# Kernel optimization log

Measured on AMD Instinct MI355X. Metric: run time of the kernel, lower is better.

The kernel has to match this reference:

```python
import jax, jax.numpy as jnp
import numpy as np

B, S, P, HID, HQ, HKV, D, MAXP = 8, 4, 4096, 4096, 32, 8, 128, 8192


def setup_inputs() -> dict:
    key = jax.random.key(0)
    ks = jax.random.split(key, 8)
    # rotary tables (Llama-style: freqs duplicated across halves)
    inv_freq = 1.0 / (10000.0 ** (jnp.arange(0, D // 2, dtype=jnp.float32) / (D // 2)))
    t = jnp.arange(MAXP, dtype=jnp.float32)
    emb = jnp.concatenate([jnp.outer(t, inv_freq)] * 2, axis=-1)  # [MAXP, D]
    w = 0.02
    return {
        "x": jax.random.normal(ks[0], (B, S, HID), dtype=jnp.float32),
        "wq": w * jax.random.normal(ks[1], (HID, HQ * D), dtype=jnp.float32),
        "wk": w * jax.random.normal(ks[2], (HID, HKV * D), dtype=jnp.float32),
        "wv": w * jax.random.normal(ks[3], (HID, HKV * D), dtype=jnp.float32),
        "wo": w * jax.random.normal(ks[4], (HQ * D, HID), dtype=jnp.float32),
        "cos": jnp.cos(emb),
        "sin": jnp.sin(emb),
        "k_cache": jax.random.normal(ks[5], (B, P, HKV, D), dtype=jnp.float32),
        "v_cache": jax.random.normal(ks[6], (B, P, HKV, D), dtype=jnp.float32),
        "past_len": P,
    }


def _rope(x, c, s):
    # x: [B,S,H,D]; c,s: [1,S,1,D] -- half-rotation RoPE
    half = x.shape[-1] // 2
    x1, x2 = x[..., :half], x[..., half:]
    return x * c + jnp.concatenate([-x2, x1], axis=-1) * s


def reference(x, wq, wk, wv, wo, cos, sin, k_cache, v_cache, past_len):
    b, s, _ = x.shape
    hq, hkv, d = HQ, HKV, D
    q = (x @ wq).reshape(b, s, hq, d)
    k = (x @ wk).reshape(b, s, hkv, d)
    v = (x @ wv).reshape(b, s, hkv, d)

    pos = past_len + jnp.arange(s)                     # new-token positions
    c = cos[pos][None, :, None, :]
    sn = sin[pos][None, :, None, :]
    q = _rope(q, c, sn)
    k = _rope(k, c, sn)

    # append new kv to cache
    k_all = jnp.concatenate([k_cache, k], axis=1)      # [B,T,HKV,D]
    v_all = jnp.concatenate([v_cache, v], axis=1)
    t_len = k_all.shape[1]

    group = hq // hkv
    qg = q.reshape(b, s, hkv, group, d)
    scores = jnp.einsum('bskgd,btkd->bkgst', qg, k_all) / jnp.sqrt(jnp.asarray(d, x.dtype))

    # causal: query at position past_len+i attends to key positions <= past_len+i
    key_pos = jnp.arange(t_len)
    mask = pos[:, None] >= key_pos[None, :]            # [S,T]
    scores = jnp.where(mask[None, None, None], scores, jnp.asarray(-1e30, scores.dtype))
    attn = jax.nn.softmax(scores, axis=-1)

    out = jnp.einsum('bkgst,btkd->bskgd', attn, v_all).reshape(b, s, hq * d)
    return out @ wo
```

## Files before the change

### kernel.cpp

```cpp
#include <hip/hip_runtime.h>
#include <math.h>

#define NB 8
#define NS 4
#define NP 4096
#define HID 4096
#define NHQ 32
#define NHKV 8
#define ND 128
#define NGROUP 4
#define NBS 32
#define NQI 16
#define NCHUNK 17
#define TCHUNK 256
#define KSPLIT 16
#define QKV_COLS 6144
#define LOG2E 1.4426950408889634f

__global__ __launch_bounds__(256) void prep_xT(const float* __restrict__ x,
                                               float* __restrict__ xT) {
  int n = blockIdx.x * 256 + threadIdx.x;
  int r = n >> 12;
  int k = n & 4095;
  xT[k * NBS + r] = x[n];
}

__global__ __launch_bounds__(256) void rope_kernel(
    const float* __restrict__ qb, const float* __restrict__ kb,
    const float* __restrict__ cosp, const float* __restrict__ sinp,
    const int* __restrict__ past_len, float* __restrict__ q_t,
    float* __restrict__ k_new) {
  int n = blockIdx.x * 256 + threadIdx.x;
  int pl = past_len[0];
  if (n < NBS * HID) {
    int r = n >> 12;
    int hd = n & 4095;
    int h = hd >> 7, d = hd & 127;
    int b = r >> 2, s = r & 3;
    int pos = pl + s;
    float c = cosp[pos * ND + d], sn = sinp[pos * ND + d];
    float v = qb[n];
    float other = (d < 64) ? -qb[n + 64] : qb[n - 64];
    float rv = fmaf(v, c, other * sn);
    int kv = h >> 2, g = h & 3;
    q_t[(((b * NHKV + kv) * ND + d) * NQI) + g * NS + s] = rv;
  } else {
    n -= NBS * HID;
    int r = n >> 10;
    int hd = n & 1023;
    int kv = hd >> 7, d = hd & 127;
    int b = r >> 2, s = r & 3;
    int pos = pl + s;
    float c = cosp[pos * ND + d], sn = sinp[pos * ND + d];
    float v = kb[n];
    float other = (d < 64) ? -kb[n + 64] : kb[n - 64];
    k_new[((b * NHKV + kv) * NS + s) * ND + d] = fmaf(v, c, other * sn);
  }
}

__global__ __launch_bounds__(256) void gemm_part(
    const float* __restrict__ A_T, const float* __restrict__ wq,
    const float* __restrict__ wk, const float* __restrict__ wv,
    const float* __restrict__ wo, float* __restrict__ P, int mode) {
  __shared__ float lds[2 * 64 * 64];
  int cb = blockIdx.x, kb = blockIdx.y;
  int ncols = mode ? 4096 : QKV_COLS;
  int col0 = cb * 128;
  const float* W;
  int ld, wcol;
  if (mode) {
    W = wo; ld = 4096; wcol = col0;
  } else if (col0 < 4096) {
    W = wq; ld = 4096; wcol = col0;
  } else if (col0 < 5120) {
    W = wk; ld = 1024; wcol = col0 - 4096;
  } else {
    W = wv; ld = 1024; wcol = col0 - 5120;
  }
  int tid = threadIdx.x;
  int lane = tid & 63;
  int wid = __builtin_amdgcn_readfirstlane(tid >> 6);
  int k0 = kb * 256 + wid * 64;
  const float* wp = W + (size_t)k0 * ld + wcol + lane * 2;
  const float* xp = A_T + (size_t)k0 * NBS;
  float acc[64];
#pragma unroll
  for (int v = 0; v < 64; v++) acc[v] = 0.f;

  float2 wbuf[8];
#pragma unroll
  for (int u = 0; u < 8; u++) wbuf[u] = *(const float2*)(wp + (size_t)u * ld);
#pragma unroll 1
  for (int kk = 0; kk < 64; kk += 8) {
    float2 cur[8];
#pragma unroll
    for (int u = 0; u < 8; u++) cur[u] = wbuf[u];
    if (kk + 8 < 64) {
#pragma unroll
      for (int u = 0; u < 8; u++)
        wbuf[u] = *(const float2*)(wp + (size_t)(kk + 8 + u) * ld);
    }
#pragma unroll
    for (int u = 0; u < 8; u++) {
      const float* xr = xp + (kk + u) * NBS;
#pragma unroll
      for (int m = 0; m < NBS; m++) {
        acc[2 * m] = fmaf(xr[m], cur[u].x, acc[2 * m]);
        acc[2 * m + 1] = fmaf(xr[m], cur[u].y, acc[2 * m + 1]);
      }
    }
  }
  if (wid >= 2) {
#pragma unroll
    for (int v = 0; v < 64; v++) lds[(wid - 2) * 4096 + v * 64 + lane] = acc[v];
  }
  __syncthreads();
  if (wid < 2) {
#pragma unroll
    for (int v = 0; v < 64; v++) acc[v] += lds[wid * 4096 + v * 64 + lane];
  }
  __syncthreads();
  if (wid == 1) {
#pragma unroll
    for (int v = 0; v < 64; v++) lds[v * 64 + lane] = acc[v];
  }
  __syncthreads();
  if (wid == 0) {
#pragma unroll
    for (int v = 0; v < 64; v++) acc[v] += lds[v * 64 + lane];
#pragma unroll
    for (int m = 0; m < NBS; m++) {
      float2 st = make_float2(acc[2 * m], acc[2 * m + 1]);
      *(float2*)(P + ((size_t)kb * NBS + m) * ncols + col0 + lane * 2) = st;
    }
  }
}

__global__ __launch_bounds__(256) void reduce_qkv(const float* __restrict__ P,
                                                  float* __restrict__ qb,
                                                  float* __restrict__ kbuf,
                                                  float* __restrict__ vbuf) {
  size_t idx = ((size_t)blockIdx.x * 256 + threadIdx.x) * 4;
  float4 s = make_float4(0.f, 0.f, 0.f, 0.f);
#pragma unroll
  for (int p = 0; p < KSPLIT; p++) {
    float4 v = *(const float4*)(P + (size_t)p * (NBS * QKV_COLS) + idx);
    s.x += v.x; s.y += v.y; s.z += v.z; s.w += v.w;
  }
  int r = (int)(idx / QKV_COLS);
  int col = (int)(idx % QKV_COLS);
  float* dst;
  if (col < 4096)
    dst = qb + (size_t)r * 4096 + col;
  else if (col < 5120)
    dst = kbuf + (size_t)r * 1024 + (col - 4096);
  else
    dst = vbuf + (size_t)r * 1024 + (col - 5120);
  *(float4*)dst = s;
}

__global__ __launch_bounds__(256) void reduce_o(const float* __restrict__ P,
                                                float* __restrict__ outp) {
  size_t idx = ((size_t)blockIdx.x * 256 + threadIdx.x) * 4;
  float4 s = make_float4(0.f, 0.f, 0.f, 0.f);
#pragma unroll
  for (int p = 0; p < KSPLIT; p++) {
    float4 v = *(const float4*)(P + (size_t)p * (NBS * 4096) + idx);
    s.x += v.x; s.y += v.y; s.z += v.z; s.w += v.w;
  }
  *(float4*)(outp + idx) = s;
}

__global__ __launch_bounds__(256) void attn_kernel(
    const float* __restrict__ q_t, const float* __restrict__ k_cache,
    const float* __restrict__ v_cache, const float* __restrict__ k_new,
    const float* __restrict__ vbuf, float* __restrict__ part_o,
    float* __restrict__ part_m, float* __restrict__ part_l) {
  __shared__ float p_lds[TCHUNK * 17];
  __shared__ float redm[NQI][4];
  __shared__ float redl[NQI][4];
  __shared__ float mfin[NQI];
  int bk = blockIdx.x;
  int chunk = blockIdx.y;
  int blk = bk * NCHUNK + chunk;
  int b = bk >> 3, kv = bk & 7;
  int tid = threadIdx.x;
  int lane = tid & 63;
  int wid = tid >> 6;
  bool last = (chunk == NCHUNK - 1);
  int tcount = last ? NS : TCHUNK;
  const float* qbase = q_t + (size_t)bk * (ND * NQI);

  int t_loc = tid;
  bool valid = t_loc < tcount;
  int t_eff = valid ? t_loc : 0;
  const float* kp =
      last ? (k_new + ((size_t)bk * NS + t_eff) * ND)
           : (k_cache +
              (((size_t)b * NP + chunk * TCHUNK + t_eff) * NHKV + kv) * ND);
  float s_acc[NQI];
#pragma unroll
  for (int i = 0; i < NQI; i++) s_acc[i] = 0.f;
#pragma unroll 8
  for (int d4 = 0; d4 < 32; ++d4) {
    float4 kvv = *(const float4*)(kp + d4 * 4);
    const float* qp = qbase + (d4 * 4) * NQI;
#pragma unroll
    for (int i = 0; i < NQI; i++) {
      float s = s_acc[i];
      s = fmaf(kvv.x, qp[i], s);
      s = fmaf(kvv.y, qp[NQI + i], s);
      s = fmaf(kvv.z, qp[2 * NQI + i], s);
      s = fmaf(kvv.w, qp[3 * NQI + i], s);
      s_acc[i] = s;
    }
  }
  const float scale = 0.08838834764831845f;
  float sc[NQI];
#pragma unroll
  for (int i = 0; i < NQI; i++) {
    float s = s_acc[i] * scale;
    if (!valid || (last && t_loc > (i & 3))) s = -__builtin_inff();
    sc[i] = s;
  }
#pragma unroll
  for (int i = 0; i < NQI; i++) {
    float m = sc[i];
#pragma unroll
    for (int off = 1; off < 64; off <<= 1) m = fmaxf(m, __shfl_xor(m, off, 64));
    if (lane == 0) redm[i][wid] = m;
  }
  __syncthreads();
  if (tid < NQI) {
    float m = fmaxf(fmaxf(redm[tid][0], redm[tid][1]),
                    fmaxf(redm[tid][2], redm[tid][3]));
    mfin[tid] = m;
  }
  __syncthreads();
  float l_loc[NQI];
#pragma unroll
  for (int i = 0; i < NQI; i++) {
    float p = exp2f((sc[i] - mfin[i]) * LOG2E);
    p_lds[t_loc * 17 + i] = p;
    l_loc[i] = p;
  }
#pragma unroll
  for (int i = 0; i < NQI; i++) {
    float l = l_loc[i];
#pragma unroll
    for (int off = 1; off < 64; off <<= 1) l += __shfl_xor(l, off, 64);
    if (lane == 0) redl[i][wid] = l;
  }
  __syncthreads();
  if (tid < NQI) {
    float l = redl[tid][0] + redl[tid][1] + redl[tid][2] + redl[tid][3];
    part_m[(size_t)blk * NQI + tid] = mfin[tid];
    part_l[(size_t)blk * NQI + tid] = l;
  }

  int r0 = tid >> 5;
  int dq = (tid & 31) * 4;
  const float* vpb =
      last ? (vbuf + (size_t)b * NS * (NHKV * ND) + kv * ND + dq)
           : (v_cache + ((size_t)b * NP + chunk * TCHUNK) * (NHKV * ND) +
              kv * ND + dq);
  float o0[4] = {0, 0, 0, 0}, o1[4] = {0, 0, 0, 0};
#pragma unroll 8
  for (int t = 0; t < tcount; ++t) {
    float4 vv = *(const float4*)(vpb + (size_t)t * (NHKV * ND));
    float p0 = p_lds[t * 17 + r0];
    float p1 = p_lds[t * 17 + r0 + 8];
    o0[0] = fmaf(p0, vv.x, o0[0]); o0[1] = fmaf(p0, vv.y, o0[1]);
    o0[2] = fmaf(p0, vv.z, o0[2]); o0[3] = fmaf(p0, vv.w, o0[3]);
    o1[0] = fmaf(p1, vv.x, o1[0]); o1[1] = fmaf(p1, vv.y, o1[1]);
    o1[2] = fmaf(p1, vv.z, o1[2]); o1[3] = fmaf(p1, vv.w, o1[3]);
  }
  size_t obase = (size_t)blk * (NQI * ND);
  *(float4*)(part_o + obase + (size_t)r0 * ND + dq) =
      make_float4(o0[0], o0[1], o0[2], o0[3]);
  *(float4*)(part_o + obase + (size_t)(r0 + 8) * ND + dq) =
      make_float4(o1[0], o1[1], o1[2], o1[3]);
}

__global__ __launch_bounds__(256) void combine_kernel(
    const float* __restrict__ part_o, const float* __restrict__ part_m,
    const float* __restrict__ part_l, float* __restrict__ attn_T) {
  int bk = blockIdx.x;
  int tid = threadIdx.x;
  int i = tid >> 4;
  int dh = (tid & 15) * 4 + blockIdx.y * 64;
  float M = -__builtin_inff();
#pragma unroll
  for (int c = 0; c < NCHUNK; c++)
    M = fmaxf(M, part_m[((size_t)bk * NCHUNK + c) * NQI + i]);
  float L = 0.f;
  float o0 = 0.f, o1 = 0.f, o2 = 0.f, o3 = 0.f;
#pragma unroll
  for (int c = 0; c < NCHUNK; c++) {
    size_t pc = (size_t)bk * NCHUNK + c;
    float mc = part_m[pc * NQI + i];
    float w = exp2f((mc - M) * LOG2E);
    L = fmaf(part_l[pc * NQI + i], w, L);
    float4 po = *(const float4*)(part_o + pc * (NQI * ND) + (size_t)i * ND + dh);
    o0 = fmaf(w, po.x, o0);
    o1 = fmaf(w, po.y, o1);
    o2 = fmaf(w, po.z, o2);
    o3 = fmaf(w, po.w, o3);
  }
  float inv = 1.0f / L;
  int b = bk >> 3, kv = bk & 7;
  int g = i >> 2, s = i & 3;
  int h = kv * NGROUP + g;
  int r = b * NS + s;
  attn_T[(size_t)(h * ND + dh + 0) * NBS + r] = o0 * inv;
  attn_T[(size_t)(h * ND + dh + 1) * NBS + r] = o1 * inv;
  attn_T[(size_t)(h * ND + dh + 2) * NBS + r] = o2 * inv;
  attn_T[(size_t)(h * ND + dh + 3) * NBS + r] = o3 * inv;
}

extern "C" void kernel_launch(void* const* d_in, const int* in_sizes, int n_in,
                              void* d_out, int out_size, void* d_ws,
                              size_t ws_size, hipStream_t stream) {
  const float* x = (const float*)d_in[0];
  const float* wq = (const float*)d_in[1];
  const float* wk = (const float*)d_in[2];
  const float* wv = (const float*)d_in[3];
  const float* wo = (const float*)d_in[4];
  const float* cosp = (const float*)d_in[5];
  const float* sinp = (const float*)d_in[6];
  const float* k_cache = (const float*)d_in[7];
  const float* v_cache = (const float*)d_in[8];
  const int* past_len = (const int*)d_in[9];
  float* out = (float*)d_out;

  float* ws = (float*)d_ws;
  float* xT = ws;
  float* qb = xT + 131072;
  float* kbuf = qb + 131072;
  float* vbuf = kbuf + 32768;
  float* q_t = vbuf + 32768;
  float* k_new = q_t + 131072;
  float* attn_T = k_new + 32768;
  float* R = attn_T + 131072;
  float* Pq = R;
  float* part_o = R;
  float* part_m = R + 2228224;
  float* part_l = part_m + 17408;
  float* Po = R;

  prep_xT<<<512, 256, 0, stream>>>(x, xT);
  gemm_part<<<dim3(48, KSPLIT), 256, 0, stream>>>(xT, wq, wk, wv, wo, Pq, 0);
  reduce_qkv<<<192, 256, 0, stream>>>(Pq, qb, kbuf, vbuf);
  rope_kernel<<<640, 256, 0, stream>>>(qb, kbuf, cosp, sinp, past_len, q_t,
                                       k_new);
  attn_kernel<<<dim3(64, NCHUNK), 256, 0, stream>>>(
      q_t, k_cache, v_cache, k_new, vbuf, part_o, part_m, part_l);
  combine_kernel<<<dim3(64, 2), 256, 0, stream>>>(part_o, part_m, part_l,
                                                  attn_T);
  gemm_part<<<dim3(32, KSPLIT), 256, 0, stream>>>(attn_T, wq, wk, wv, wo, Po,
                                                  1);
  reduce_o<<<128, 256, 0, stream>>>(Po, out);
}
```

Before: 463.2 us.

## Stage GEMM activations in LDS, widen weight loads, split attention PV over time

The split-K GEMM now copies its activation slice into shared memory and has each lane load float4 weight columns (4 columns by 16 rows instead of 2 by 32). It also doubles the K-split to 32 when the workspace is large enough, which adds parallelism but doubles the partial-sum traffic seen by the reduce kernels. The attention PV stage now gives each warp a 32-token slice and all 16 queries, with a transposed P layout, followed by a cross-warp reduction in LDS. This trades more accumulator registers and extra syncs for fewer redundant V reads.

```diff
diff --git a/kernel.cpp b/kernel.cpp
--- a/kernel.cpp
+++ b/kernel.cpp
@@ -13,7 +13,6 @@
 #define NQI 16
 #define NCHUNK 17
 #define TCHUNK 256
-#define KSPLIT 16
 #define QKV_COLS 6144
 #define LOG2E 1.4426950408889634f
 
@@ -58,11 +57,12 @@
   }
 }
 
+template <int KSLICE>
 __global__ __launch_bounds__(256) void gemm_part(
     const float* __restrict__ A_T, const float* __restrict__ wq,
     const float* __restrict__ wk, const float* __restrict__ wv,
     const float* __restrict__ wo, float* __restrict__ P, int mode) {
-  __shared__ float lds[2 * 64 * 64];
+  __shared__ __align__(16) float lds[8192];
   int cb = blockIdx.x, kb = blockIdx.y;
   int ncols = mode ? 4096 : QKV_COLS;
   int col0 = cb * 128;
@@ -80,36 +80,62 @@
   int tid = threadIdx.x;
   int lane = tid & 63;
   int wid = __builtin_amdgcn_readfirstlane(tid >> 6);
-  int k0 = kb * 256 + wid * 64;
-  const float* wp = W + (size_t)k0 * ld + wcol + lane * 2;
-  const float* xp = A_T + (size_t)k0 * NBS;
+  int l32 = lane & 31;
+  int mh = lane >> 5;
+  int kblk = kb * KSLICE;
+  constexpr int KW = KSLICE / 4;
+  int k0 = wid * KW;
+  const float* wp = W + (size_t)(kblk + k0) * ld + wcol + l32 * 4;
+
+  float4 wb[8];
+#pragma unroll
+  for (int u = 0; u < 8; u++) wb[u] = *(const float4*)(wp + (size_t)u * ld);
+
+  {
+    const float4* src = (const float4*)(A_T + (size_t)kblk * NBS);
+    float4* dst = (float4*)lds;
+#pragma unroll
+    for (int p = 0; p < KSLICE / 32; p++)
+      dst[p * 256 + tid] = src[p * 256 + tid];
+  }
+  __syncthreads();
+
   float acc[64];
 #pragma unroll
   for (int v = 0; v < 64; v++) acc[v] = 0.f;
 
-  float2 wbuf[8];
-#pragma unroll
-  for (int u = 0; u < 8; u++) wbuf[u] = *(const float2*)(wp + (size_t)u * ld);
-#pragma unroll 1
-  for (int kk = 0; kk < 64; kk += 8) {
-    float2 cur[8];
-#pragma unroll
-    for (int u = 0; u < 8; u++) cur[u] = wbuf[u];
-    if (kk + 8 < 64) {
-#pragma unroll
-      for (int u = 0; u < 8; u++)
-        wbuf[u] = *(const float2*)(wp + (size_t)(kk + 8 + u) * ld);
-    }
-#pragma unroll
-    for (int u = 0; u < 8; u++) {
-      const float* xr = xp + (kk + u) * NBS;
-#pragma unroll
-      for (int m = 0; m < NBS; m++) {
-        acc[2 * m] = fmaf(xr[m], cur[u].x, acc[2 * m]);
-        acc[2 * m + 1] = fmaf(xr[m], cur[u].y, acc[2 * m + 1]);
-      }
-    }
-  }
+  const float* xp = lds + (size_t)k0 * NBS + mh * 16;
+
+  auto body = [&](int kk, float4 w) {
+    const float* xr = xp + (size_t)kk * NBS;
+    float4 xa = *(const float4*)(xr);
+    float4 xb = *(const float4*)(xr + 4);
+    float4 xc = *(const float4*)(xr + 8);
+    float4 xd = *(const float4*)(xr + 12);
+    float xm[16] = {xa.x, xa.y, xa.z, xa.w, xb.x, xb.y, xb.z, xb.w,
+                    xc.x, xc.y, xc.z, xc.w, xd.x, xd.y, xd.z, xd.w};
+#pragma unroll
+    for (int m = 0; m < 16; m++) {
+      acc[4 * m + 0] = fmaf(xm[m], w.x, acc[4 * m + 0]);
+      acc[4 * m + 1] = fmaf(xm[m], w.y, acc[4 * m + 1]);
+      acc[4 * m + 2] = fmaf(xm[m], w.z, acc[4 * m + 2]);
+      acc[4 * m + 3] = fmaf(xm[m], w.w, acc[4 * m + 3]);
+    }
+  };
+
+#pragma unroll 8
+  for (int kk = 0; kk < KW - 8; kk++) {
+    float4 w = wb[kk & 7];
+    wb[kk & 7] = *(const float4*)(wp + (size_t)(kk + 8) * ld);
+    body(kk, w);
+  }
+#pragma unroll
+  for (int kk = KW - 8; kk < KW; kk++) {
+    float4 w = wb[kk & 7];
+    body(kk, w);
+  }
+
+  __syncthreads();
   if (wid >= 2) {
 #pragma unroll
     for (int v = 0; v < 64; v++) lds[(wid - 2) * 4096 + v * 64 + lane] = acc[v];
@@ -129,13 +155,16 @@
 #pragma unroll
     for (int v = 0; v < 64; v++) acc[v] += lds[v * 64 + lane];
 #pragma unroll
-    for (int m = 0; m < NBS; m++) {
-      float2 st = make_float2(acc[2 * m], acc[2 * m + 1]);
-      *(float2*)(P + ((size_t)kb * NBS + m) * ncols + col0 + lane * 2) = st;
-    }
-  }
-}
-
+    for (int m = 0; m < 16; m++) {
+      float4 st = make_float4(acc[4 * m], acc[4 * m + 1], acc[4 * m + 2],
+                              acc[4 * m + 3]);
+      *(float4*)(P + ((size_t)kb * NBS + mh * 16 + m) * ncols + col0 +
+                 l32 * 4) = st;
+    }
+  }
+}
+
+template <int KS>
 __global__ __launch_bounds__(256) void reduce_qkv(const float* __restrict__ P,
                                                   float* __restrict__ qb,
                                                   float* __restrict__ kbuf,
@@ -143,7 +172,7 @@
   size_t idx = ((size_t)blockIdx.x * 256 + threadIdx.x) * 4;
   float4 s = make_float4(0.f, 0.f, 0.f, 0.f);
 #pragma unroll
-  for (int p = 0; p < KSPLIT; p++) {
+  for (int p = 0; p < KS; p++) {
     float4 v = *(const float4*)(P + (size_t)p * (NBS * QKV_COLS) + idx);
     s.x += v.x; s.y += v.y; s.z += v.z; s.w += v.w;
   }
@@ -159,12 +188,13 @@
   *(float4*)dst = s;
 }
 
+template <int KS>
 __global__ __launch_bounds__(256) void reduce_o(const float* __restrict__ P,
                                                 float* __restrict__ outp) {
   size_t idx = ((size_t)blockIdx.x * 256 + threadIdx.x) * 4;
   float4 s = make_float4(0.f, 0.f, 0.f, 0.f);
 #pragma unroll
-  for (int p = 0; p < KSPLIT; p++) {
+  for (int p = 0; p < KS; p++) {
     float4 v = *(const float4*)(P + (size_t)p * (NBS * 4096) + idx);
     s.x += v.x; s.y += v.y; s.z += v.z; s.w += v.w;
   }
@@ -176,10 +206,11 @@
     const float* __restrict__ v_cache, const float* __restrict__ k_new,
     const float* __restrict__ vbuf, float* __restrict__ part_o,
     float* __restrict__ part_m, float* __restrict__ part_l) {
-  __shared__ float p_lds[TCHUNK * 17];
+  __shared__ __align__(16) float sbuf[NQI * TCHUNK];
   __shared__ float redm[NQI][4];
   __shared__ float redl[NQI][4];
   __shared__ float mfin[NQI];
+  float* p_lds = sbuf;
   int bk = blockIdx.x;
   int chunk = blockIdx.y;
   int blk = bk * NCHUNK + chunk;
@@ -232,16 +263,15 @@
   }
   __syncthreads();
   if (tid < NQI) {
-    float m = fmaxf(fmaxf(redm[tid][0], redm[tid][1]),
-                    fmaxf(redm[tid][2], redm[tid][3]));
-    mfin[tid] = m;
+    mfin[tid] = fmaxf(fmaxf(redm[tid][0], redm[tid][1]),
+                      fmaxf(redm[tid][2], redm[tid][3]));
   }
   __syncthreads();
   float l_loc[NQI];
 #pragma unroll
   for (int i = 0; i < NQI; i++) {
     float p = exp2f((sc[i] - mfin[i]) * LOG2E);
-    p_lds[t_loc * 17 + i] = p;
+    p_lds[i * TCHUNK + t_loc] = p;
     l_loc[i] = p;
   }
 #pragma unroll
@@ -253,33 +283,75 @@
   }
   __syncthreads();
   if (tid < NQI) {
-    float l = redl[tid][0] + redl[tid][1] + redl[tid][2] + redl[tid][3];
     part_m[(size_t)blk * NQI + tid] = mfin[tid];
-    part_l[(size_t)blk * NQI + tid] = l;
-  }
-
-  int r0 = tid >> 5;
+    part_l[(size_t)blk * NQI + tid] =
+        redl[tid][0] + redl[tid][1] + redl[tid][2] + redl[tid][3];
+  }
+
+  int g = tid >> 5;
   int dq = (tid & 31) * 4;
+  int tbeg = g * 32;
+  int tnum = tcount - tbeg;
+  tnum = tnum < 0 ? 0 : (tnum > 32 ? 32 : tnum);
   const float* vpb =
-      last ? (vbuf + (size_t)b * NS * (NHKV * ND) + kv * ND + dq)
-           : (v_cache + ((size_t)b * NP + chunk * TCHUNK) * (NHKV * ND) +
+      last ? (vbuf + ((size_t)b * NS + tbeg) * (NHKV * ND) + kv * ND + dq)
+           : (v_cache + ((size_t)b * NP + chunk * TCHUNK + tbeg) * (NHKV * ND) +
               kv * ND + dq);
-  float o0[4] = {0, 0, 0, 0}, o1[4] = {0, 0, 0, 0};
-#pragma unroll 8
-  for (int t = 0; t < tcount; ++t) {
-    float4 vv = *(const float4*)(vpb + (size_t)t * (NHKV * ND));
-    float p0 = p_lds[t * 17 + r0];
-    float p1 = p_lds[t * 17 + r0 + 8];
-    o0[0] = fmaf(p0, vv.x, o0[0]); o0[1] = fmaf(p0, vv.y, o0[1]);
-    o0[2] = fmaf(p0, vv.z, o0[2]); o0[3] = fmaf(p0, vv.w, o0[3]);
-    o1[0] = fmaf(p1, vv.x, o1[0]); o1[1] = fmaf(p1, vv.y, o1[1]);
-    o1[2] = fmaf(p1, vv.z, o1[2]); o1[3] = fmaf(p1, vv.w, o1[3]);
-  }
-  size_t obase = (size_t)blk * (NQI * ND);
-  *(float4*)(part_o + obase + (size_t)r0 * ND + dq) =
-      make_float4(o0[0], o0[1], o0[2], o0[3]);
-  *(float4*)(part_o + obase + (size_t)(r0 + 8) * ND + dq) =
-      make_float4(o1[0], o1[1], o1[2], o1[3]);
+  float o[NQI][4];
+#pragma unroll
+  for (int i = 0; i < NQI; i++) o[i][0] = o[i][1] = o[i][2] = o[i][3] = 0.f;
+#pragma unroll 4
+  for (int tt = 0; tt < tnum; ++tt) {
+    float4 vv = *(const float4*)(vpb + (size_t)tt * (NHKV * ND));
+    const float* pp = p_lds + (tbeg + tt);
+#pragma unroll
+    for (int i = 0; i < NQI; i++) {
+      float p = pp[i * TCHUNK];
+      o[i][0] = fmaf(p, vv.x, o[i][0]);
+      o[i][1] = fmaf(p, vv.y, o[i][1]);
+      o[i][2] = fmaf(p, vv.z, o[i][2]);
+      o[i][3] = fmaf(p, vv.w, o[i][3]);
+    }
+  }
+#pragma unroll
+  for (int i = 0; i < NQI; i++) {
+#pragma unroll
+    for (int c = 0; c < 4; c++) o[i][c] += __shfl_xor(o[i][c], 32, 64);
+  }
+  __syncthreads();
+  float* red = sbuf;
+  if (wid >= 2 && lane < 32) {
+#pragma unroll
+    for (int i = 0; i < NQI; i++)
+      *(float4*)(red + ((wid - 2) * NQI + i) * 128 + dq) =
+          make_float4(o[i][0], o[i][1], o[i][2], o[i][3]);
+  }
+  __syncthreads();
+  if (wid < 2 && lane < 32) {
+#pragma unroll
+    for (int i = 0; i < NQI; i++) {
+      float4 r = *(const float4*)(red + (wid * NQI + i) * 128 + dq);
+      o[i][0] += r.x; o[i][1] += r.y; o[i][2] += r.z; o[i][3] += r.w;
+    }
+  }
+  __syncthreads();
+  if (wid == 1 && lane < 32) {
+#pragma unroll
+    for (int i = 0; i < NQI; i++)
+      *(float4*)(red + i * 128 + dq) =
+          make_float4(o[i][0], o[i][1], o[i][2], o[i][3]);
+  }
+  __syncthreads();
+  if (wid == 0 && lane < 32) {
+    size_t obase = (size_t)blk * (NQI * ND);
+#pragma unroll
+    for (int i = 0; i < NQI; i++) {
+      float4 r = *(const float4*)(red + i * 128 + dq);
+      *(float4*)(part_o + obase + (size_t)i * ND + dq) =
+          make_float4(o[i][0] + r.x, o[i][1] + r.y, o[i][2] + r.z,
+                      o[i][3] + r.w);
+    }
+  }
 }
 
 __global__ __launch_bounds__(256) void combine_kernel(
@@ -348,16 +420,30 @@
   float* part_l = part_m + 17408;
   float* Po = R;
 
+  const size_t need32 = (size_t)(622592 + 32 * NBS * QKV_COLS) * sizeof(float);
+  const bool big = ws_size >= need32;
+
   prep_xT<<<512, 256, 0, stream>>>(x, xT);
-  gemm_part<<<dim3(48, KSPLIT), 256, 0, stream>>>(xT, wq, wk, wv, wo, Pq, 0);
-  reduce_qkv<<<192, 256, 0, stream>>>(Pq, qb, kbuf, vbuf);
+  if (big) {
+    gemm_part<128><<<dim3(48, 32), 256, 0, stream>>>(xT, wq, wk, wv, wo, Pq, 0);
+    reduce_qkv<32><<<192, 256, 0, stream>>>(Pq, qb, kbuf, vbuf);
+  } else {
+    gemm_part<256><<<dim3(48, 16), 256, 0, stream>>>(xT, wq, wk, wv, wo, Pq, 0);
+    reduce_qkv<16><<<192, 256, 0, stream>>>(Pq, qb, kbuf, vbuf);
+  }
   rope_kernel<<<640, 256, 0, stream>>>(qb, kbuf, cosp, sinp, past_len, q_t,
                                        k_new);
   attn_kernel<<<dim3(64, NCHUNK), 256, 0, stream>>>(
       q_t, k_cache, v_cache, k_new, vbuf, part_o, part_m, part_l);
   combine_kernel<<<dim3(64, 2), 256, 0, stream>>>(part_o, part_m, part_l,
                                                   attn_T);
-  gemm_part<<<dim3(32, KSPLIT), 256, 0, stream>>>(attn_T, wq, wk, wv, wo, Po,
-                                                  1);
-  reduce_o<<<128, 256, 0, stream>>>(Po, out);
-}
+  if (big) {
+    gemm_part<128><<<dim3(32, 32), 256, 0, stream>>>(attn_T, wq, wk, wv, wo,
+                                                     Po, 1);
+    reduce_o<32><<<128, 256, 0, stream>>>(Po, out);
+  } else {
+    gemm_part<256><<<dim3(32, 16), 256, 0, stream>>>(attn_T, wq, wk, wv, wo,
+                                                     Po, 1);
+    reduce_o<16><<<128, 256, 0, stream>>>(Po, out);
+  }
+}
```

Result: no change. 464.6 us (+0.3%).

## Restructure skinny GEMM with async global-to-LDS double-buffered weight tiles

Applied to the files above, without the earlier changes.

Rewrites the split-K GEMM so each block covers 256 columns and a K slice. Weight rows stream into a double-buffered LDS tile through global_load_lds, and the activations are staged once in LDS. Each wave now owns 8 rows by 4 columns, which removes the cross-wave LDS reduction. A deeper split-K (32 slices) is used when the workspace is large enough. The intent is better bandwidth use on the weight stream and more blocks in flight, at the cost of larger partial buffers and a longer reduce.

```diff
diff --git a/kernel.cpp b/kernel.cpp
--- a/kernel.cpp
+++ b/kernel.cpp
@@ -13,7 +13,6 @@
 #define NQI 16
 #define NCHUNK 17
 #define TCHUNK 256
-#define KSPLIT 16
 #define QKV_COLS 6144
 #define LOG2E 1.4426950408889634f
 
@@ -58,14 +57,23 @@
   }
 }
 
+__device__ __forceinline__ void gl_lds16(const float* g, float* l) {
+  __builtin_amdgcn_global_load_lds(
+      (const __attribute__((address_space(1))) void*)g,
+      (__attribute__((address_space(3))) void*)l, 16, 0, 0);
+}
+
+template <int KSLICE>
 __global__ __launch_bounds__(256) void gemm_part(
     const float* __restrict__ A_T, const float* __restrict__ wq,
     const float* __restrict__ wk, const float* __restrict__ wv,
     const float* __restrict__ wo, float* __restrict__ P, int mode) {
-  __shared__ float lds[2 * 64 * 64];
+  constexpr int NCH = KSLICE / 16;
+  __shared__ __align__(16) float xs[KSLICE * 32];
+  __shared__ __align__(16) float wbuf[2 * 16 * 256];
   int cb = blockIdx.x, kb = blockIdx.y;
   int ncols = mode ? 4096 : QKV_COLS;
-  int col0 = cb * 128;
+  int col0 = cb * 256;
   const float* W;
   int ld, wcol;
   if (mode) {
@@ -80,62 +88,80 @@
   int tid = threadIdx.x;
   int lane = tid & 63;
   int wid = __builtin_amdgcn_readfirstlane(tid >> 6);
-  int k0 = kb * 256 + wid * 64;
-  const float* wp = W + (size_t)k0 * ld + wcol + lane * 2;
-  const float* xp = A_T + (size_t)k0 * NBS;
-  float acc[64];
-#pragma unroll
-  for (int v = 0; v < 64; v++) acc[v] = 0.f;
-
-  float2 wbuf[8];
-#pragma unroll
-  for (int u = 0; u < 8; u++) wbuf[u] = *(const float2*)(wp + (size_t)u * ld);
+  int lane4 = lane * 4;
+  int m0 = wid * 8;
+  int kblk = kb * KSLICE;
+  const float* wbase = W + (size_t)kblk * ld + wcol;
+
+#pragma unroll
+  for (int j = 0; j < KSLICE / 32; j++) {
+    gl_lds16(A_T + (size_t)kblk * 32 + j * 1024 + wid * 256 + lane4,
+             xs + j * 1024 + wid * 256);
+  }
+#pragma unroll
+  for (int j = 0; j < 4; j++) {
+    int row = j * 4 + wid;
+    gl_lds16(wbase + (size_t)row * ld + lane4, wbuf + row * 256);
+  }
+#pragma unroll
+  for (int j = 0; j < 4; j++) {
+    int row = j * 4 + wid;
+    gl_lds16(wbase + (size_t)(16 + row) * ld + lane4,
+             wbuf + 4096 + row * 256);
+  }
+
+  float acc[8][4];
+#pragma unroll
+  for (int m = 0; m < 8; m++)
+    acc[m][0] = acc[m][1] = acc[m][2] = acc[m][3] = 0.f;
+
 #pragma unroll 1
-  for (int kk = 0; kk < 64; kk += 8) {
-    float2 cur[8];
-#pragma unroll
-    for (int u = 0; u < 8; u++) cur[u] = wbuf[u];
-    if (kk + 8 < 64) {
-#pragma unroll
-      for (int u = 0; u < 8; u++)
-        wbuf[u] = *(const float2*)(wp + (size_t)(kk + 8 + u) * ld);
-    }
-#pragma unroll
-    for (int u = 0; u < 8; u++) {
-      const float* xr = xp + (kk + u) * NBS;
-#pragma unroll
-      for (int m = 0; m < NBS; m++) {
-        acc[2 * m] = fmaf(xr[m], cur[u].x, acc[2 * m]);
-        acc[2 * m + 1] = fmaf(xr[m], cur[u].y, acc[2 * m + 1]);
+  for (int c = 0; c < NCH; c++) {
+    if (c < NCH - 1)
+      asm volatile("s_waitcnt vmcnt(4)" ::: "memory");
+    else
+      asm volatile("s_waitcnt vmcnt(0)" ::: "memory");
+    __builtin_amdgcn_s_barrier();
+    asm volatile("" ::: "memory");
+
+    const float* wbp = wbuf + (c & 1) * 4096;
+    const float* xcp = xs + c * 512 + m0;
+#pragma unroll
+    for (int k = 0; k < 16; k++) {
+      float4 w4 = *(const float4*)(wbp + k * 256 + lane4);
+      const float* xr = xcp + k * 32;
+      float4 xa = *(const float4*)(xr);
+      float4 xb = *(const float4*)(xr + 4);
+      float xm[8] = {xa.x, xa.y, xa.z, xa.w, xb.x, xb.y, xb.z, xb.w};
+#pragma unroll
+      for (int m = 0; m < 8; m++) {
+        acc[m][0] = fmaf(xm[m], w4.x, acc[m][0]);
+        acc[m][1] = fmaf(xm[m], w4.y, acc[m][1]);
+        acc[m][2] = fmaf(xm[m], w4.z, acc[m][2]);
+        acc[m][3] = fmaf(xm[m], w4.w, acc[m][3]);
       }
     }
-  }
-  if (wid >= 2) {
-#pragma unroll
-    for (int v = 0; v < 64; v++) lds[(wid - 2) * 4096 + v * 64 + lane] = acc[v];
-  }
-  __syncthreads();
-  if (wid < 2) {
-#pragma unroll
-    for (int v = 0; v < 64; v++) acc[v] += lds[wid * 4096 + v * 64 + lane];
-  }
-  __syncthreads();
-  if (wid == 1) {
-#pragma unroll
-    for (int v = 0; v < 64; v++) lds[v * 64 + lane] = acc[v];
-  }
-  __syncthreads();
-  if (wid == 0) {
-#pragma unroll
-    for (int v = 0; v < 64; v++) acc[v] += lds[v * 64 + lane];
-#pragma unroll
-    for (int m = 0; m < NBS; m++) {
-      float2 st = make_float2(acc[2 * m], acc[2 * m + 1]);
-      *(float2*)(P + ((size_t)kb * NBS + m) * ncols + col0 + lane * 2) = st;
+
+    asm volatile("" ::: "memory");
+    __builtin_amdgcn_s_barrier();
+    if (c + 2 < NCH) {
+#pragma unroll
+      for (int j = 0; j < 4; j++) {
+        int row = j * 4 + wid;
+        gl_lds16(wbase + (size_t)((c + 2) * 16 + row) * ld + lane4,
+                 wbuf + (c & 1) * 4096 + row * 256);
+      }
     }
   }
-}
-
+
+#pragma unroll
+  for (int m = 0; m < 8; m++) {
+    *(float4*)(P + ((size_t)kb * NBS + m0 + m) * ncols + col0 + lane4) =
+        make_float4(acc[m][0], acc[m][1], acc[m][2], acc[m][3]);
+  }
+}
+
+template <int KS>
 __global__ __launch_bounds__(256) void reduce_qkv(const float* __restrict__ P,
                                                   float* __restrict__ qb,
                                                   float* __restrict__ kbuf,
@@ -143,7 +169,7 @@
   size_t idx = ((size_t)blockIdx.x * 256 + threadIdx.x) * 4;
   float4 s = make_float4(0.f, 0.f, 0.f, 0.f);
 #pragma unroll
-  for (int p = 0; p < KSPLIT; p++) {
+  for (int p = 0; p < KS; p++) {
     float4 v = *(const float4*)(P + (size_t)p * (NBS * QKV_COLS) + idx);
     s.x += v.x; s.y += v.y; s.z += v.z; s.w += v.w;
   }
@@ -159,12 +185,13 @@
   *(float4*)dst = s;
 }
 
+template <int KS>
 __global__ __launch_bounds__(256) void reduce_o(const float* __restrict__ P,
                                                 float* __restrict__ outp) {
   size_t idx = ((size_t)blockIdx.x * 256 + threadIdx.x) * 4;
   float4 s = make_float4(0.f, 0.f, 0.f, 0.f);
 #pragma unroll
-  for (int p = 0; p < KSPLIT; p++) {
+  for (int p = 0; p < KS; p++) {
     float4 v = *(const float4*)(P + (size_t)p * (NBS * 4096) + idx);
     s.x += v.x; s.y += v.y; s.z += v.z; s.w += v.w;
   }
@@ -348,16 +375,30 @@
   float* part_l = part_m + 17408;
   float* Po = R;
 
+  const size_t need32 = (size_t)(622592 + 32 * NBS * QKV_COLS) * sizeof(float);
+  const bool big = ws_size >= need32;
+
   prep_xT<<<512, 256, 0, stream>>>(x, xT);
-  gemm_part<<<dim3(48, KSPLIT), 256, 0, stream>>>(xT, wq, wk, wv, wo, Pq, 0);
-  reduce_qkv<<<192, 256, 0, stream>>>(Pq, qb, kbuf, vbuf);
+  if (big) {
+    gemm_part<128><<<dim3(24, 32), 256, 0, stream>>>(xT, wq, wk, wv, wo, Pq, 0);
+    reduce_qkv<32><<<192, 256, 0, stream>>>(Pq, qb, kbuf, vbuf);
+  } else {
+    gemm_part<256><<<dim3(24, 16), 256, 0, stream>>>(xT, wq, wk, wv, wo, Pq, 0);
+    reduce_qkv<16><<<192, 256, 0, stream>>>(Pq, qb, kbuf, vbuf);
+  }
   rope_kernel<<<640, 256, 0, stream>>>(qb, kbuf, cosp, sinp, past_len, q_t,
                                        k_new);
   attn_kernel<<<dim3(64, NCHUNK), 256, 0, stream>>>(
       q_t, k_cache, v_cache, k_new, vbuf, part_o, part_m, part_l);
   combine_kernel<<<dim3(64, 2), 256, 0, stream>>>(part_o, part_m, part_l,
                                                   attn_T);
-  gemm_part<<<dim3(32, KSPLIT), 256, 0, stream>>>(attn_T, wq, wk, wv, wo, Po,
-                                                  1);
-  reduce_o<<<128, 256, 0, stream>>>(Po, out);
-}
+  if (big) {
+    gemm_part<128><<<dim3(16, 32), 256, 0, stream>>>(attn_T, wq, wk, wv, wo,
+                                                     Po, 1);
+    reduce_o<32><<<128, 256, 0, stream>>>(Po, out);
+  } else {
+    gemm_part<256><<<dim3(16, 16), 256, 0, stream>>>(attn_T, wq, wk, wv, wo,
+                                                     Po, 1);
+    reduce_o<16><<<128, 256, 0, stream>>>(Po, out);
+  }
+}
```

Result: faster. 452.0 us (-2.4%).

## Fuse pre/post attention stages into persistent kernels with grid barriers and LDS-staged GEMM

Applied to the files above, without the earlier changes.

Merges the transpose, QKV GEMM, split-K reduction and RoPE into one persistent kernel, and merges combine, output GEMM and reduction into another, using atomic grid-wide barriers. This cuts the number of launches from eight to three. The GEMM now stages x and weight tiles into LDS through global_load_lds with double buffering, and each wave owns 8 rows instead of doing a cross-wave LDS reduction. RoPE is fused into the split-K reduction by exchanging the rotated half through LDS. The grid barriers rely on all 768 blocks being co-resident, which risks deadlock if occupancy is too low, and they add atomic spin overhead.

```diff
diff --git a/kernel.cpp b/kernel.cpp
--- a/kernel.cpp
+++ b/kernel.cpp
@@ -13,162 +13,164 @@
 #define NQI 16
 #define NCHUNK 17
 #define TCHUNK 256
+#define QKV_COLS 6144
 #define KSPLIT 16
-#define QKV_COLS 6144
+#define KSLICE 256
+#define GRID_PRE 768
 #define LOG2E 1.4426950408889634f
 
-__global__ __launch_bounds__(256) void prep_xT(const float* __restrict__ x,
-                                               float* __restrict__ xT) {
-  int n = blockIdx.x * 256 + threadIdx.x;
-  int r = n >> 12;
-  int k = n & 4095;
-  xT[k * NBS + r] = x[n];
-}
-
-__global__ __launch_bounds__(256) void rope_kernel(
-    const float* __restrict__ qb, const float* __restrict__ kb,
-    const float* __restrict__ cosp, const float* __restrict__ sinp,
-    const int* __restrict__ past_len, float* __restrict__ q_t,
-    float* __restrict__ k_new) {
-  int n = blockIdx.x * 256 + threadIdx.x;
-  int pl = past_len[0];
-  if (n < NBS * HID) {
-    int r = n >> 12;
-    int hd = n & 4095;
-    int h = hd >> 7, d = hd & 127;
-    int b = r >> 2, s = r & 3;
-    int pos = pl + s;
-    float c = cosp[pos * ND + d], sn = sinp[pos * ND + d];
-    float v = qb[n];
-    float other = (d < 64) ? -qb[n + 64] : qb[n - 64];
-    float rv = fmaf(v, c, other * sn);
-    int kv = h >> 2, g = h & 3;
-    q_t[(((b * NHKV + kv) * ND + d) * NQI) + g * NS + s] = rv;
-  } else {
-    n -= NBS * HID;
-    int r = n >> 10;
-    int hd = n & 1023;
-    int kv = hd >> 7, d = hd & 127;
-    int b = r >> 2, s = r & 3;
-    int pos = pl + s;
-    float c = cosp[pos * ND + d], sn = sinp[pos * ND + d];
-    float v = kb[n];
-    float other = (d < 64) ? -kb[n + 64] : kb[n - 64];
-    k_new[((b * NHKV + kv) * NS + s) * ND + d] = fmaf(v, c, other * sn);
-  }
-}
-
-__global__ __launch_bounds__(256) void gemm_part(
-    const float* __restrict__ A_T, const float* __restrict__ wq,
-    const float* __restrict__ wk, const float* __restrict__ wv,
-    const float* __restrict__ wo, float* __restrict__ P, int mode) {
-  __shared__ float lds[2 * 64 * 64];
-  int cb = blockIdx.x, kb = blockIdx.y;
-  int ncols = mode ? 4096 : QKV_COLS;
-  int col0 = cb * 128;
-  const float* W;
-  int ld, wcol;
-  if (mode) {
-    W = wo; ld = 4096; wcol = col0;
-  } else if (col0 < 4096) {
-    W = wq; ld = 4096; wcol = col0;
-  } else if (col0 < 5120) {
-    W = wk; ld = 1024; wcol = col0 - 4096;
-  } else {
-    W = wv; ld = 1024; wcol = col0 - 5120;
-  }
+__device__ __forceinline__ void gl_lds16(const float* g, float* l) {
+  __builtin_amdgcn_global_load_lds(
+      (const __attribute__((address_space(1))) void*)g,
+      (__attribute__((address_space(3))) void*)l, 16, 0, 0);
+}
+
+__device__ __forceinline__ void gsync(unsigned* arrive, unsigned* release,
+                                      unsigned gen, int nblk) {
+  __syncthreads();
+  if (threadIdx.x == 0) {
+    __threadfence();
+    unsigned old = atomicAdd(arrive, 1u);
+    if (old == (unsigned)(nblk - 1)) {
+      atomicExch(arrive, 0u);
+      __threadfence();
+      atomicAdd(release, 1u);
+    } else {
+      while (atomicAdd(release, 0u) < gen) __builtin_amdgcn_s_sleep(2);
+    }
+    __threadfence();
+  }
+  __syncthreads();
+}
+
+__device__ __forceinline__ void gemm_stage(const float* __restrict__ A_T,
+                                           const float* __restrict__ Wc,
+                                           int ld, float* __restrict__ P,
+                                           int ncols, int col0, int kb,
+                                           float* xs, float* wbuf) {
   int tid = threadIdx.x;
   int lane = tid & 63;
   int wid = __builtin_amdgcn_readfirstlane(tid >> 6);
-  int k0 = kb * 256 + wid * 64;
-  const float* wp = W + (size_t)k0 * ld + wcol + lane * 2;
-  const float* xp = A_T + (size_t)k0 * NBS;
-  float acc[64];
-#pragma unroll
-  for (int v = 0; v < 64; v++) acc[v] = 0.f;
-
-  float2 wbuf[8];
-#pragma unroll
-  for (int u = 0; u < 8; u++) wbuf[u] = *(const float2*)(wp + (size_t)u * ld);
+  int kblk = kb * KSLICE;
+  const float* wbase = Wc + (size_t)kblk * ld;
+  int wrow = 2 * wid + (lane >> 5);
+  int wcol = (lane & 31) * 4;
+  const float* wsrc = wbase + (size_t)wrow * ld + wcol;
+
+#pragma unroll
+  for (int j = 0; j < 8; j++) {
+    int off = wid * 2048 + j * 256;
+    gl_lds16(A_T + (size_t)kblk * NBS + off + lane * 4, xs + off);
+  }
+  gl_lds16(wsrc, wbuf + wrow * 128);
+  gl_lds16(wsrc + (size_t)8 * ld, wbuf + 1024 + wrow * 128);
+
+  float acc[8][2];
+#pragma unroll
+  for (int m = 0; m < 8; m++) acc[m][0] = acc[m][1] = 0.f;
+
+  constexpr int NCH = KSLICE / 8;
 #pragma unroll 1
-  for (int kk = 0; kk < 64; kk += 8) {
-    float2 cur[8];
-#pragma unroll
-    for (int u = 0; u < 8; u++) cur[u] = wbuf[u];
-    if (kk + 8 < 64) {
-#pragma unroll
-      for (int u = 0; u < 8; u++)
-        wbuf[u] = *(const float2*)(wp + (size_t)(kk + 8 + u) * ld);
-    }
-#pragma unroll
-    for (int u = 0; u < 8; u++) {
-      const float* xr = xp + (kk + u) * NBS;
-#pragma unroll
-      for (int m = 0; m < NBS; m++) {
-        acc[2 * m] = fmaf(xr[m], cur[u].x, acc[2 * m]);
-        acc[2 * m + 1] = fmaf(xr[m], cur[u].y, acc[2 * m + 1]);
+  for (int c = 0; c < NCH; c++) {
+    if (c < NCH - 1)
+      asm volatile("s_waitcnt vmcnt(1)" ::: "memory");
+    else
+      asm volatile("s_waitcnt vmcnt(0)" ::: "memory");
+    __builtin_amdgcn_s_barrier();
+    asm volatile("" ::: "memory");
+
+    const float* wbp = wbuf + (c & 1) * 1024;
+    const float* xcp = xs + c * 256 + wid * 8;
+#pragma unroll
+    for (int k = 0; k < 8; k++) {
+      float2 w2 = *(const float2*)(wbp + k * 128 + lane * 2);
+      float4 xa = *(const float4*)(xcp + k * 32);
+      float4 xb = *(const float4*)(xcp + k * 32 + 4);
+      float xm[8] = {xa.x, xa.y, xa.z, xa.w, xb.x, xb.y, xb.z, xb.w};
+#pragma unroll
+      for (int m = 0; m < 8; m++) {
+        acc[m][0] = fmaf(xm[m], w2.x, acc[m][0]);
+        acc[m][1] = fmaf(xm[m], w2.y, acc[m][1]);
       }
     }
-  }
-  if (wid >= 2) {
-#pragma unroll
-    for (int v = 0; v < 64; v++) lds[(wid - 2) * 4096 + v * 64 + lane] = acc[v];
-  }
-  __syncthreads();
-  if (wid < 2) {
-#pragma unroll
-    for (int v = 0; v < 64; v++) acc[v] += lds[wid * 4096 + v * 64 + lane];
-  }
-  __syncthreads();
-  if (wid == 1) {
-#pragma unroll
-    for (int v = 0; v < 64; v++) lds[v * 64 + lane] = acc[v];
-  }
-  __syncthreads();
-  if (wid == 0) {
-#pragma unroll
-    for (int v = 0; v < 64; v++) acc[v] += lds[v * 64 + lane];
-#pragma unroll
-    for (int m = 0; m < NBS; m++) {
-      float2 st = make_float2(acc[2 * m], acc[2 * m + 1]);
-      *(float2*)(P + ((size_t)kb * NBS + m) * ncols + col0 + lane * 2) = st;
-    }
-  }
-}
-
-__global__ __launch_bounds__(256) void reduce_qkv(const float* __restrict__ P,
-                                                  float* __restrict__ qb,
-                                                  float* __restrict__ kbuf,
-                                                  float* __restrict__ vbuf) {
-  size_t idx = ((size_t)blockIdx.x * 256 + threadIdx.x) * 4;
-  float4 s = make_float4(0.f, 0.f, 0.f, 0.f);
-#pragma unroll
-  for (int p = 0; p < KSPLIT; p++) {
-    float4 v = *(const float4*)(P + (size_t)p * (NBS * QKV_COLS) + idx);
-    s.x += v.x; s.y += v.y; s.z += v.z; s.w += v.w;
-  }
-  int r = (int)(idx / QKV_COLS);
-  int col = (int)(idx % QKV_COLS);
-  float* dst;
-  if (col < 4096)
-    dst = qb + (size_t)r * 4096 + col;
-  else if (col < 5120)
-    dst = kbuf + (size_t)r * 1024 + (col - 4096);
-  else
-    dst = vbuf + (size_t)r * 1024 + (col - 5120);
-  *(float4*)dst = s;
-}
-
-__global__ __launch_bounds__(256) void reduce_o(const float* __restrict__ P,
-                                                float* __restrict__ outp) {
-  size_t idx = ((size_t)blockIdx.x * 256 + threadIdx.x) * 4;
-  float4 s = make_float4(0.f, 0.f, 0.f, 0.f);
-#pragma unroll
-  for (int p = 0; p < KSPLIT; p++) {
-    float4 v = *(const float4*)(P + (size_t)p * (NBS * 4096) + idx);
-    s.x += v.x; s.y += v.y; s.z += v.z; s.w += v.w;
-  }
-  *(float4*)(outp + idx) = s;
+
+    asm volatile("" ::: "memory");
+    __builtin_amdgcn_s_barrier();
+    if (c + 2 < NCH)
+      gl_lds16(wsrc + (size_t)((c + 2) * 8) * ld,
+               wbuf + (c & 1) * 1024 + wrow * 128);
+  }
+
+#pragma unroll
+  for (int m = 0; m < 8; m++)
+    *(float2*)(P + ((size_t)kb * NBS + wid * 8 + m) * ncols + col0 +
+               lane * 2) = make_float2(acc[m][0], acc[m][1]);
+}
+
+__global__ __launch_bounds__(256, 4) void k_pre(
+    const float* __restrict__ x, const float* __restrict__ wq,
+    const float* __restrict__ wk, const float* __restrict__ wv,
+    const float* __restrict__ cosp, const float* __restrict__ sinp,
+    const int* __restrict__ past_len, float* __restrict__ xT,
+    float* __restrict__ Pq, float* __restrict__ q_t,
+    float* __restrict__ k_new, float* __restrict__ vbuf,
+    unsigned* __restrict__ bar) {
+  __shared__ __align__(16) float lds[KSLICE * NBS + 2 * 8 * 128];
+  int bid = blockIdx.x;
+  int tid = threadIdx.x;
+  int gid = bid * 256 + tid;
+
+  if (gid < NBS * HID) {
+    int r = gid >> 12, k = gid & 4095;
+    xT[k * NBS + r] = x[gid];
+  }
+  gsync(bar, bar + 1, 1, GRID_PRE);
+
+  {
+    int cb = bid >> 4, kb = bid & 15;
+    int col0 = cb * 128;
+    const float* Wc;
+    int ld;
+    if (col0 < 4096) {
+      Wc = wq + col0; ld = 4096;
+    } else if (col0 < 5120) {
+      Wc = wk + (col0 - 4096); ld = 1024;
+    } else {
+      Wc = wv + (col0 - 5120); ld = 1024;
+    }
+    gemm_stage(xT, Wc, ld, Pq, QKV_COLS, col0, kb, lds, lds + KSLICE * NBS);
+  }
+  gsync(bar, bar + 1, 2, GRID_PRE);
+
+  {
+    float s = 0.f;
+#pragma unroll
+    for (int p = 0; p < KSPLIT; p++)
+      s += Pq[(size_t)p * (NBS * QKV_COLS) + gid];
+    lds[tid] = s;
+    __syncthreads();
+    float other = lds[tid ^ 64];
+    int r = gid / QKV_COLS;
+    int col = gid - r * QKV_COLS;
+    int b = r >> 2, si = r & 3;
+    int pos = past_len[0] + si;
+    if (col < 4096) {
+      int h = col >> 7, d = col & 127;
+      float c = cosp[pos * ND + d], sn = sinp[pos * ND + d];
+      float oth = (d < 64) ? -other : other;
+      int kv = h >> 2, g = h & 3;
+      q_t[(((b * NHKV + kv) * ND + d) * NQI) + g * NS + si] =
+          fmaf(s, c, oth * sn);
+    } else if (col < 5120) {
+      int cc = col - 4096;
+      int kv = cc >> 7, d = cc & 127;
+      float c = cosp[pos * ND + d], sn = sinp[pos * ND + d];
+      float oth = (d < 64) ? -other : other;
+      k_new[((b * NHKV + kv) * NS + si) * ND + d] = fmaf(s, c, oth * sn);
+    } else {
+      vbuf[(size_t)r * 1024 + (col - 5120)] = s;
+    }
+  }
 }
 
 __global__ __launch_bounds__(256) void attn_kernel(
@@ -282,40 +284,66 @@
       make_float4(o1[0], o1[1], o1[2], o1[3]);
 }
 
-__global__ __launch_bounds__(256) void combine_kernel(
+__global__ __launch_bounds__(256, 4) void k_post(
     const float* __restrict__ part_o, const float* __restrict__ part_m,
-    const float* __restrict__ part_l, float* __restrict__ attn_T) {
-  int bk = blockIdx.x;
-  int tid = threadIdx.x;
-  int i = tid >> 4;
-  int dh = (tid & 15) * 4 + blockIdx.y * 64;
-  float M = -__builtin_inff();
-#pragma unroll
-  for (int c = 0; c < NCHUNK; c++)
-    M = fmaxf(M, part_m[((size_t)bk * NCHUNK + c) * NQI + i]);
-  float L = 0.f;
-  float o0 = 0.f, o1 = 0.f, o2 = 0.f, o3 = 0.f;
-#pragma unroll
-  for (int c = 0; c < NCHUNK; c++) {
-    size_t pc = (size_t)bk * NCHUNK + c;
-    float mc = part_m[pc * NQI + i];
-    float w = exp2f((mc - M) * LOG2E);
-    L = fmaf(part_l[pc * NQI + i], w, L);
-    float4 po = *(const float4*)(part_o + pc * (NQI * ND) + (size_t)i * ND + dh);
-    o0 = fmaf(w, po.x, o0);
-    o1 = fmaf(w, po.y, o1);
-    o2 = fmaf(w, po.z, o2);
-    o3 = fmaf(w, po.w, o3);
-  }
-  float inv = 1.0f / L;
-  int b = bk >> 3, kv = bk & 7;
-  int g = i >> 2, s = i & 3;
-  int h = kv * NGROUP + g;
-  int r = b * NS + s;
-  attn_T[(size_t)(h * ND + dh + 0) * NBS + r] = o0 * inv;
-  attn_T[(size_t)(h * ND + dh + 1) * NBS + r] = o1 * inv;
-  attn_T[(size_t)(h * ND + dh + 2) * NBS + r] = o2 * inv;
-  attn_T[(size_t)(h * ND + dh + 3) * NBS + r] = o3 * inv;
+    const float* __restrict__ part_l, const float* __restrict__ wo,
+    float* __restrict__ attn_T, float* __restrict__ Po,
+    float* __restrict__ out, unsigned* __restrict__ bar) {
+  __shared__ __align__(16) float lds[KSLICE * NBS + 2 * 8 * 128];
+  int bid = blockIdx.x, tid = threadIdx.x;
+  int gid = bid * 256 + tid;
+
+  if (gid < 32768) {
+    int bk = gid >> 9;
+    int i = (gid >> 5) & 15;
+    int dh = (gid & 31) * 4;
+    float M = -__builtin_inff();
+#pragma unroll
+    for (int c = 0; c < NCHUNK; c++)
+      M = fmaxf(M, part_m[((size_t)bk * NCHUNK + c) * NQI + i]);
+    float L = 0.f, o0 = 0.f, o1 = 0.f, o2 = 0.f, o3 = 0.f;
+#pragma unroll
+    for (int c = 0; c < NCHUNK; c++) {
+      size_t pc = (size_t)bk * NCHUNK + c;
+      float w = exp2f((part_m[pc * NQI + i] - M) * LOG2E);
+      L = fmaf(part_l[pc * NQI + i], w, L);
+      float4 po =
+          *(const float4*)(part_o + pc * (NQI * ND) + (size_t)i * ND + dh);
+      o0 = fmaf(w, po.x, o0);
+      o1 = fmaf(w, po.y, o1);
+      o2 = fmaf(w, po.z, o2);
+      o3 = fmaf(w, po.w, o3);
+    }
+    float inv = 1.0f / L;
+    int b = bk >> 3, kv = bk & 7;
+    int g = i >> 2, si = i & 3;
+    int h = kv * NGROUP + g;
+    int r = b * NS + si;
+    attn_T[(size_t)(h * ND + dh + 0) * NBS + r] = o0 * inv;
+    attn_T[(size_t)(h * ND + dh + 1) * NBS + r] = o1 * inv;
+    attn_T[(size_t)(h * ND + dh + 2) * NBS + r] = o2 * inv;
+    attn_T[(size_t)(h * ND + dh + 3) * NBS + r] = o3 * inv;
+  }
+  gsync(bar, bar + 1, 1, GRID_PRE);
+
+  if (bid < 512) {
+    int cb = bid >> 4, kb = bid & 15;
+    int col0 = cb * 128;
+    gemm_stage(attn_T, wo + col0, 4096, Po, 4096, col0, kb, lds,
+               lds + KSLICE * NBS);
+  }
+  gsync(bar, bar + 1, 2, GRID_PRE);
+
+  if (gid < 32768) {
+    size_t idx = (size_t)gid * 4;
+    float4 s4 = make_float4(0.f, 0.f, 0.f, 0.f);
+#pragma unroll
+    for (int p = 0; p < KSPLIT; p++) {
+      float4 v = *(const float4*)(Po + (size_t)p * (NBS * 4096) + idx);
+      s4.x += v.x; s4.y += v.y; s4.z += v.z; s4.w += v.w;
+    }
+    *(float4*)(out + idx) = s4;
+  }
 }
 
 extern "C" void kernel_launch(void* const* d_in, const int* in_sizes, int n_in,
@@ -335,29 +363,23 @@
 
   float* ws = (float*)d_ws;
   float* xT = ws;
-  float* qb = xT + 131072;
-  float* kbuf = qb + 131072;
-  float* vbuf = kbuf + 32768;
-  float* q_t = vbuf + 32768;
+  float* q_t = xT + 131072;
   float* k_new = q_t + 131072;
-  float* attn_T = k_new + 32768;
-  float* R = attn_T + 131072;
+  float* vbuf = k_new + 32768;
+  float* attn_T = vbuf + 32768;
+  unsigned* bar = (unsigned*)(attn_T + 131072);
+  float* R = attn_T + 131072 + 16;
   float* Pq = R;
   float* part_o = R;
   float* part_m = R + 2228224;
   float* part_l = part_m + 17408;
   float* Po = R;
 
-  prep_xT<<<512, 256, 0, stream>>>(x, xT);
-  gemm_part<<<dim3(48, KSPLIT), 256, 0, stream>>>(xT, wq, wk, wv, wo, Pq, 0);
-  reduce_qkv<<<192, 256, 0, stream>>>(Pq, qb, kbuf, vbuf);
-  rope_kernel<<<640, 256, 0, stream>>>(qb, kbuf, cosp, sinp, past_len, q_t,
-                                       k_new);
+  hipMemsetAsync(bar, 0, 16, stream);
+  k_pre<<<GRID_PRE, 256, 0, stream>>>(x, wq, wk, wv, cosp, sinp, past_len, xT,
+                                      Pq, q_t, k_new, vbuf, bar);
   attn_kernel<<<dim3(64, NCHUNK), 256, 0, stream>>>(
       q_t, k_cache, v_cache, k_new, vbuf, part_o, part_m, part_l);
-  combine_kernel<<<dim3(64, 2), 256, 0, stream>>>(part_o, part_m, part_l,
-                                                  attn_T);
-  gemm_part<<<dim3(32, KSPLIT), 256, 0, stream>>>(attn_T, wq, wk, wv, wo, Po,
-                                                  1);
-  reduce_o<<<128, 256, 0, stream>>>(Po, out);
-}
+  k_post<<<GRID_PRE, 256, 0, stream>>>(part_o, part_m, part_l, wo, attn_T, Po,
+                                       out, bar + 2);
+}
```

Measured after the change: 715.9 us. 54.5% more time.
